# Kernel tuning notes

Measured on AMD Instinct MI355X. Metric: run time of the kernel, lower is better.

The kernel has to match this reference:

```python
import jax, jax.numpy as jnp
import numpy as np

NUM_HEADS = 16
EMBED = 1024
HEAD_DIM = EMBED // NUM_HEADS


def setup_inputs() -> dict:
    key = jax.random.key(0)
    k1, k2, k3, k4, k5 = jax.random.split(key, 5)
    B, N, D = 16, 1024, EMBED
    s_in = 1.0 / np.sqrt(D)
    x = jax.random.normal(k1, (B, N, D), dtype=jnp.float32)
    # Linear weights stored as [in, out] so y = x @ W + b (equiv to torch x @ W.T + b)
    W_qkv = jax.random.uniform(k2, (D, 3 * D), dtype=jnp.float32, minval=-s_in, maxval=s_in)
    b_qkv = jax.random.uniform(k3, (3 * D,), dtype=jnp.float32, minval=-s_in, maxval=s_in)
    W_fc = jax.random.uniform(k4, (D, D), dtype=jnp.float32, minval=-s_in, maxval=s_in)
    b_fc = jax.random.uniform(k5, (D,), dtype=jnp.float32, minval=-s_in, maxval=s_in)
    return {"x": x, "W_qkv": W_qkv, "b_qkv": b_qkv, "W_fc": W_fc, "b_fc": b_fc}


def reference(x, W_qkv, b_qkv, W_fc, b_fc):
    B, N, D = x.shape
    H, d_k = NUM_HEADS, HEAD_DIM
    qkv = x @ W_qkv + b_qkv                      # [B, N, 3D]
    qkv = qkv.reshape(B, N, 3, H, d_k)
    qkv = jnp.transpose(qkv, (2, 0, 3, 1, 4))    # [3, B, H, N, d_k]
    Q, K, V = qkv[0], qkv[1], qkv[2]
    scale = 1.0 / jnp.sqrt(jnp.asarray(d_k, dtype=x.dtype))
    scores = jnp.einsum("bhqd,bhkd->bhqk", Q, K) * scale
    attn = jax.nn.softmax(scores, axis=-1)       # dropout is identity in eval mode
    context = jnp.einsum("bhqk,bhkd->bhqd", attn, V)
    context = jnp.transpose(context, (0, 2, 1, 3)).reshape(B, N, D)
    return context @ W_fc + b_fc
```

## Files before the change

### kernel.cpp

```cpp
#include <hip/hip_runtime.h>
#include <cstdint>
#include <cstddef>

typedef unsigned short u16;
typedef __bf16 bf16_t;
typedef bf16_t bf16x8 __attribute__((ext_vector_type(8)));
typedef float f32x4 __attribute__((ext_vector_type(4)));

#define MFMA16(a, b, c) __builtin_amdgcn_mfma_f32_16x16x32_bf16((a), (b), (c), 0, 0, 0)
#define GLOBAL_AS __attribute__((address_space(1)))
#define LDS_AS __attribute__((address_space(3)))

#define SOFT_M 8.0f

__device__ __forceinline__ u16 f2bf(float f) {
    unsigned u = __float_as_uint(f);
    u += 0x7FFFu + ((u >> 16) & 1u);
    return (u16)(u >> 16);
}
__device__ __forceinline__ u16 f2bf_trunc(float f) {
    return (u16)(__float_as_uint(f) >> 16);
}
__device__ __forceinline__ void gll16(const u16* g, u16* l) {
    __builtin_amdgcn_global_load_lds((const GLOBAL_AS unsigned int*)g,
                                     (LDS_AS unsigned int*)l, 16, 0, 0);
}

__global__ __launch_bounds__(256) void conv_x_kernel(const float* __restrict__ x,
                                                     u16* __restrict__ xb) {
    int i = blockIdx.x * 256 + threadIdx.x;
    float4 v = ((const float4*)x)[i];
    ushort4 o;
    o.x = f2bf(v.x); o.y = f2bf(v.y); o.z = f2bf(v.z); o.w = f2bf(v.w);
    ((ushort4*)xb)[i] = o;
}

__global__ __launch_bounds__(256) void transpose_w_kernel(const float* __restrict__ W,
                                                          u16* __restrict__ Wt,
                                                          int R, int C) {
    __shared__ u16 tile[32][33];
    int c0 = blockIdx.x * 32, r0 = blockIdx.y * 32;
    int tx = threadIdx.x, ty = threadIdx.y;
#pragma unroll
    for (int i = 0; i < 4; i++)
        tile[ty + i * 8][tx] = f2bf(W[(size_t)(r0 + ty + i * 8) * C + c0 + tx]);
    __syncthreads();
#pragma unroll
    for (int i = 0; i < 4; i++)
        Wt[(size_t)(c0 + ty + i * 8) * R + r0 + tx] = tile[tx][ty + i * 8];
}

template <bool PROJ>
__global__ __launch_bounds__(512, 2) void gemm256_kernel(const u16* __restrict__ A,
                                                         const u16* __restrict__ Bt,
                                                         const float* __restrict__ bias,
                                                         u16* __restrict__ Qb,
                                                         u16* __restrict__ Kb,
                                                         u16* __restrict__ Vt,
                                                         float* __restrict__ outF) {
    __shared__ u16 lds[65536];
    u16* ldsA = lds;
    u16* ldsB = lds + 32768;

    int t = threadIdx.x;
    int lane = t & 63, wid = t >> 6;
    int lr = lane & 15, quad = lane >> 4;
    int m0 = blockIdx.x * 256, n0 = blockIdx.y * 256;
    int wmBase = (wid >> 2) * 128;
    int wnBase = (wid & 3) * 64;
    int kcol = (quad * 8) ^ (((lr >> 1) & 3) << 3);

    int srow = wid * 16 + (lane >> 2);
    int schk = ((lane & 3) ^ ((lane >> 3) & 3)) * 8;
    const u16* AgT = A + (size_t)(m0 + srow) * 1024 + schk;
    const u16* BgT = Bt + (size_t)(n0 + srow) * 1024 + schk;
    int dstOff = wid * 512;

    auto stageA = [&](int tt) {
        u16* d = ldsA + (tt & 3) * 8192 + dstOff;
        const u16* s = AgT + (size_t)tt * 32;
        gll16(s, d);
        gll16(s + 131072, d + 4096);
    };
    auto stageB = [&](int tt) {
        u16* d = ldsB + (tt & 3) * 8192 + dstOff;
        const u16* s = BgT + (size_t)tt * 32;
        gll16(s, d);
        gll16(s + 131072, d + 4096);
    };

    f32x4 acc[8][4];
    f32x4 zf = {0.f, 0.f, 0.f, 0.f};
#pragma unroll
    for (int i = 0; i < 8; i++)
#pragma unroll
        for (int j = 0; j < 4; j++) acc[i][j] = zf;

    stageA(0); stageB(0);
    stageA(1); stageB(1);
    asm volatile("s_waitcnt vmcnt(4)" ::: "memory");
    __builtin_amdgcn_s_barrier();
    __builtin_amdgcn_sched_barrier(0);

#pragma unroll 1
    for (int kt = 0; kt < 32; ++kt) {
        const u16* SA = ldsA + (kt & 3) * 8192;
        const u16* SB = ldsB + (kt & 3) * 8192;
        bf16x8 af[8];
#pragma unroll
        for (int mt = 0; mt < 8; mt++)
            af[mt] = *(const bf16x8*)&SA[(wmBase + mt * 16 + lr) * 32 + kcol];
        bf16x8 b0 = *(const bf16x8*)&SB[(wnBase + lr) * 32 + kcol];
        bf16x8 b1 = *(const bf16x8*)&SB[(wnBase + 16 + lr) * 32 + kcol];
        if (kt < 30) stageA(kt + 2);
        __builtin_amdgcn_s_barrier();
        __builtin_amdgcn_s_setprio(1);
#pragma unroll
        for (int mt = 0; mt < 8; mt++) {
            acc[mt][0] = MFMA16(af[mt], b0, acc[mt][0]);
            acc[mt][1] = MFMA16(af[mt], b1, acc[mt][1]);
        }
        __builtin_amdgcn_s_setprio(0);
        __builtin_amdgcn_s_barrier();
        bf16x8 b2 = *(const bf16x8*)&SB[(wnBase + 32 + lr) * 32 + kcol];
        bf16x8 b3 = *(const bf16x8*)&SB[(wnBase + 48 + lr) * 32 + kcol];
        if (kt < 30) stageB(kt + 2);
        __builtin_amdgcn_s_barrier();
        __builtin_amdgcn_s_setprio(1);
#pragma unroll
        for (int mt = 0; mt < 8; mt++) {
            acc[mt][2] = MFMA16(af[mt], b2, acc[mt][2]);
            acc[mt][3] = MFMA16(af[mt], b3, acc[mt][3]);
        }
        __builtin_amdgcn_s_setprio(0);
        if (kt <= 29)      asm volatile("s_waitcnt vmcnt(4)" ::: "memory");
        else if (kt == 30) asm volatile("s_waitcnt vmcnt(0)" ::: "memory");
        __builtin_amdgcn_s_barrier();
        __builtin_amdgcn_sched_barrier(0);
    }

    if constexpr (PROJ) {
#pragma unroll
        for (int nt = 0; nt < 4; nt++) {
            int col = n0 + wnBase + nt * 16 + lr;
            float bv = bias[col];
#pragma unroll
            for (int mt = 0; mt < 8; mt++) {
                f32x4 v = acc[mt][nt];
#pragma unroll
                for (int r = 0; r < 4; r++) {
                    int m = m0 + wmBase + mt * 16 + quad * 4 + r;
                    outF[(size_t)m * 1024 + col] = v[r] + bv;
                }
            }
        }
    } else {
        int s = n0 >> 10;
        if (s == 2) {
#pragma unroll
            for (int nt = 0; nt < 4; nt++) {
                int col = n0 + wnBase + nt * 16 + lr;
                int h = (col >> 6) & 15, d = col & 63;
                float bv = bias[col];
                int dsw = (d & 7) << 3;
#pragma unroll
                for (int mt = 0; mt < 8; mt++) {
                    f32x4 v = acc[mt][nt];
                    int mb = m0 + wmBase + mt * 16 + quad * 4;
                    int bb = mb >> 10, nn = mb & 1023;
                    int nn2 = (nn & ~63) | ((nn & 63) ^ dsw);
                    ushort4 o;
                    o.x = f2bf(v[0] + bv); o.y = f2bf(v[1] + bv);
                    o.z = f2bf(v[2] + bv); o.w = f2bf(v[3] + bv);
                    *(ushort4*)&Vt[(((size_t)(bb * 16 + h)) * 64 + d) * 1024 + nn2] = o;
                }
            }
        } else {
            u16* dst = (s == 0) ? Qb : Kb;
            float scale = (s == 0) ? 0.125f * 1.44269504089f : 1.0f;
#pragma unroll
            for (int nt = 0; nt < 4; nt++) {
                int col = n0 + wnBase + nt * 16 + lr;
                int h = (col >> 6) & 15, d = col & 63;
                float bv = bias[col];
#pragma unroll
                for (int mt = 0; mt < 8; mt++) {
                    f32x4 v = acc[mt][nt];
#pragma unroll
                    for (int r = 0; r < 4; r++) {
                        int m = m0 + wmBase + mt * 16 + quad * 4 + r;
                        int bb = m >> 10, nn = m & 1023;
                        int d2 = (s == 1) ? (d ^ ((nn & 7) << 3)) : d;
                        dst[(((size_t)(bb * 16 + h)) * 1024 + nn) * 64 + d2] =
                            f2bf((v[r] + bv) * scale);
                    }
                }
            }
        }
    }
}

__device__ __forceinline__ uint4 build_pa(f32x4 s0, f32x4 s1, float& lacc, bool qodd) {
    unsigned w[4];
    float part = 0.f;
#pragma unroll
    for (int half = 0; half < 2; half++) {
        unsigned lo = f2bf_trunc(__builtin_amdgcn_exp2f(s0[half * 2] - SOFT_M));
        unsigned hi = f2bf_trunc(__builtin_amdgcn_exp2f(s0[half * 2 + 1] - SOFT_M));
        part += __uint_as_float(lo << 16) + __uint_as_float(hi << 16);
        w[half] = lo | (hi << 16);
    }
#pragma unroll
    for (int half = 0; half < 2; half++) {
        unsigned lo = f2bf_trunc(__builtin_amdgcn_exp2f(s1[half * 2] - SOFT_M));
        unsigned hi = f2bf_trunc(__builtin_amdgcn_exp2f(s1[half * 2 + 1] - SOFT_M));
        part += __uint_as_float(lo << 16) + __uint_as_float(hi << 16);
        w[2 + half] = lo | (hi << 16);
    }
    lacc += part;
    unsigned x0 = qodd ? w[0] : w[2];
    unsigned x1 = qodd ? w[1] : w[3];
    unsigned y0 = __shfl_xor(x0, 16);
    unsigned y1 = __shfl_xor(x1, 16);
    uint4 r;
    r.x = qodd ? y0 : w[0];
    r.y = qodd ? y1 : w[1];
    r.z = qodd ? w[2] : y0;
    r.w = qodd ? w[3] : y1;
    return r;
}

__global__ __launch_bounds__(256, 4) void flash_attn_kernel(const u16* __restrict__ Qb,
                                                            const u16* __restrict__ Kb,
                                                            const u16* __restrict__ Vt,
                                                            u16* __restrict__ ctx) {
    __shared__ u16 smem[16384];
    u16* Ks0 = smem;
    u16* Vs0 = smem + 8192;
    int t = threadIdx.x, lane = t & 63, wid = t >> 6;
    int lr = lane & 15, quad = lane >> 4;
    int bh = blockIdx.x, q0 = blockIdx.y * 128;
    int b = bh >> 4, h = bh & 15;
    int xsw = (lr & 7) << 3;

    const u16* Kg = Kb + (size_t)bh * 65536;
    const u16* Vg = Vt + (size_t)bh * 65536;

#pragma unroll
    for (int i = 0; i < 2; i++) {
        gll16(Kg + wid * 1024 + i * 512 + lane * 8, Ks0 + wid * 1024 + i * 512);
        int row = wid * 16 + i * 8 + (lane >> 3);
        gll16(Vg + (size_t)row * 1024 + (lane & 7) * 8, Vs0 + wid * 1024 + i * 512);
    }

    const u16* Qw = Qb + ((size_t)bh * 1024 + q0 + wid * 32) * 64;
    bf16x8 qf[2][2];
#pragma unroll
    for (int mt = 0; mt < 2; mt++)
#pragma unroll
        for (int kk = 0; kk < 2; kk++)
            qf[mt][kk] = *(const bf16x8*)(Qw + (mt * 16 + lr) * 64 + kk * 32 + quad * 8);

    f32x4 oacc[2][4];
    f32x4 zf = {0.f, 0.f, 0.f, 0.f};
#pragma unroll
    for (int mt = 0; mt < 2; mt++)
#pragma unroll
        for (int dt = 0; dt < 4; dt++) oacc[mt][dt] = zf;
    float lsum0 = 0.f, lsum1 = 0.f;
    bool qodd = (quad & 1) != 0;
    int vperm8 = (((quad & 1) << 1) | (quad >> 1)) * 8;

    __syncthreads();

    for (int kt = 0; kt < 16; kt++) {
        int cur = kt & 1;
        if (kt < 15) {
            u16* kd = Ks0 + (cur ^ 1) * 4096;
            u16* vd = Vs0 + (cur ^ 1) * 4096;
            const u16* ks = Kg + (size_t)(kt + 1) * 4096;
#pragma unroll
            for (int i = 0; i < 2; i++) {
                gll16(ks + wid * 1024 + i * 512 + lane * 8, kd + wid * 1024 + i * 512);
                int row = wid * 16 + i * 8 + (lane >> 3);
                gll16(Vg + (size_t)row * 1024 + (kt + 1) * 64 + (lane & 7) * 8,
                      vd + wid * 1024 + i * 512);
            }
        }

        const u16* Kc = Ks0 + cur * 4096;
        f32x4 sc[2][4];
#pragma unroll
        for (int mt = 0; mt < 2; mt++)
#pragma unroll
            for (int nt = 0; nt < 4; nt++) sc[mt][nt] = zf;
#pragma unroll
        for (int nt = 0; nt < 4; nt++) {
            bf16x8 kf0 = *(const bf16x8*)&Kc[(nt * 16 + lr) * 64 + ((quad * 8) ^ xsw)];
            bf16x8 kf1 = *(const bf16x8*)&Kc[(nt * 16 + lr) * 64 + ((quad * 8 + 32) ^ xsw)];
#pragma unroll
            for (int mt = 0; mt < 2; mt++) {
                sc[mt][nt] = MFMA16(kf0, qf[mt][0], sc[mt][nt]);
                sc[mt][nt] = MFMA16(kf1, qf[mt][1], sc[mt][nt]);
            }
        }

        const u16* Vc = Vs0 + cur * 4096;
#pragma unroll
        for (int kc = 0; kc < 2; kc++) {
            uint4 pw0 = build_pa(sc[0][kc * 2], sc[0][kc * 2 + 1], lsum0, qodd);
            uint4 pw1 = build_pa(sc[1][kc * 2], sc[1][kc * 2 + 1], lsum1, qodd);
            bf16x8 pa0 = *(const bf16x8*)&pw0;
            bf16x8 pa1 = *(const bf16x8*)&pw1;
#pragma unroll
            for (int dt = 0; dt < 4; dt++) {
                bf16x8 vv = *(const bf16x8*)&Vc[(dt * 16 + lr) * 64 +
                                                ((kc * 32 + vperm8) ^ xsw)];
                oacc[0][dt] = MFMA16(pa0, vv, oacc[0][dt]);
                oacc[1][dt] = MFMA16(pa1, vv, oacc[1][dt]);
            }
        }

        __syncthreads();
    }

    u16* Ow = smem + wid * 2304;
#pragma unroll
    for (int mt = 0; mt < 2; mt++) {
        float lf = (mt == 0) ? lsum0 : lsum1;
        lf += __shfl_xor(lf, 16);
        lf += __shfl_xor(lf, 32);
        float inv = 1.0f / lf;
#pragma unroll
        for (int r = 0; r < 4; r++) {
            float invr = __shfl(inv, (lane & 48) | (quad * 4 + r));
#pragma unroll
            for (int dt = 0; dt < 4; dt++)
                Ow[(mt * 16 + quad * 4 + r) * 72 + dt * 16 + lr] =
                    f2bf(oacc[mt][dt][r] * invr);
        }
    }
#pragma unroll
    for (int j = 0; j < 4; j++) {
        int r2 = j * 8 + (lane >> 3);
        uint4 ov = *(const uint4*)&Ow[r2 * 72 + (lane & 7) * 8];
        int row = q0 + wid * 32 + r2;
        *(uint4*)&ctx[((size_t)b * 1024 + row) * 1024 + h * 64 + (lane & 7) * 8] = ov;
    }
}

extern "C" void kernel_launch(void* const* d_in, const int* in_sizes, int n_in,
                              void* d_out, int out_size, void* d_ws, size_t ws_size,
                              hipStream_t stream) {
    const float* x     = (const float*)d_in[0];
    const float* W_qkv = (const float*)d_in[1];
    const float* b_qkv = (const float*)d_in[2];
    const float* W_fc  = (const float*)d_in[3];
    const float* b_fc  = (const float*)d_in[4];
    float* out = (float*)d_out;
    char* ws = (char*)d_ws;

    u16* xb  = (u16*)(ws + 0);
    u16* wqt = (u16*)(ws + 33554432);
    u16* wft = (u16*)(ws + 39845888);
    u16* Qb  = (u16*)(ws + 41943040);
    u16* Kb  = (u16*)(ws + 75497472);
    u16* Vt  = (u16*)(ws + 109051904);
    u16* ctx = (u16*)(ws + 0);

    conv_x_kernel<<<16384, 256, 0, stream>>>(x, xb);
    transpose_w_kernel<<<dim3(96, 32), dim3(32, 8), 0, stream>>>(W_qkv, wqt, 1024, 3072);
    transpose_w_kernel<<<dim3(32, 32), dim3(32, 8), 0, stream>>>(W_fc, wft, 1024, 1024);
    gemm256_kernel<false><<<dim3(64, 12), 512, 0, stream>>>(xb, wqt, b_qkv,
                                                            Qb, Kb, Vt, nullptr);
    flash_attn_kernel<<<dim3(256, 8), 256, 0, stream>>>(Qb, Kb, Vt, ctx);
    gemm256_kernel<true><<<dim3(64, 4), 512, 0, stream>>>(ctx, wft, b_fc,
                                                          nullptr, nullptr, nullptr, out);
}
```

Measured before the change: 391.4 us.

## Deepen GEMM LDS prefetch to three stages and use one barrier per k-step

The bf16 GEMM main loop now keeps three k-tiles of global-to-LDS loads in flight instead of two, issuing both A and B stages for tile kt+3 at the top of each iteration. The split into two half-MFMA phases separated by three barriers is replaced by loading all four B fragments at once, running all 32 MFMAs, then one wait and one barrier per iteration. The vmcnt wait thresholds are adjusted to match the deeper ring. This aims to hide more global memory latency and cut synchronisation overhead, at the cost of more outstanding loads and slightly more register pressure for the extra B fragments.

```diff
diff --git a/kernel.cpp b/kernel.cpp
--- a/kernel.cpp
+++ b/kernel.cpp
@@ -98,42 +98,35 @@
 
     stageA(0); stageB(0);
     stageA(1); stageB(1);
-    asm volatile("s_waitcnt vmcnt(4)" ::: "memory");
+    stageA(2); stageB(2);
+    asm volatile("s_waitcnt vmcnt(8)" ::: "memory");
     __builtin_amdgcn_s_barrier();
     __builtin_amdgcn_sched_barrier(0);
 
 #pragma unroll 1
     for (int kt = 0; kt < 32; ++kt) {
+        if (kt <= 28) { stageA(kt + 3); stageB(kt + 3); }
+
         const u16* SA = ldsA + (kt & 3) * 8192;
         const u16* SB = ldsB + (kt & 3) * 8192;
-        bf16x8 af[8];
+        bf16x8 af[8], bfr[4];
 #pragma unroll
         for (int mt = 0; mt < 8; mt++)
             af[mt] = *(const bf16x8*)&SA[(wmBase + mt * 16 + lr) * 32 + kcol];
-        bf16x8 b0 = *(const bf16x8*)&SB[(wnBase + lr) * 32 + kcol];
-        bf16x8 b1 = *(const bf16x8*)&SB[(wnBase + 16 + lr) * 32 + kcol];
-        if (kt < 30) stageA(kt + 2);
-        __builtin_amdgcn_s_barrier();
+#pragma unroll
+        for (int nt = 0; nt < 4; nt++)
+            bfr[nt] = *(const bf16x8*)&SB[(wnBase + nt * 16 + lr) * 32 + kcol];
+
         __builtin_amdgcn_s_setprio(1);
 #pragma unroll
-        for (int mt = 0; mt < 8; mt++) {
-            acc[mt][0] = MFMA16(af[mt], b0, acc[mt][0]);
-            acc[mt][1] = MFMA16(af[mt], b1, acc[mt][1]);
-        }
+        for (int mt = 0; mt < 8; mt++)
+#pragma unroll
+            for (int nt = 0; nt < 4; nt++)
+                acc[mt][nt] = MFMA16(af[mt], bfr[nt], acc[mt][nt]);
         __builtin_amdgcn_s_setprio(0);
-        __builtin_amdgcn_s_barrier();
-        bf16x8 b2 = *(const bf16x8*)&SB[(wnBase + 32 + lr) * 32 + kcol];
-        bf16x8 b3 = *(const bf16x8*)&SB[(wnBase + 48 + lr) * 32 + kcol];
-        if (kt < 30) stageB(kt + 2);
-        __builtin_amdgcn_s_barrier();
-        __builtin_amdgcn_s_setprio(1);
-#pragma unroll
-        for (int mt = 0; mt < 8; mt++) {
-            acc[mt][2] = MFMA16(af[mt], b2, acc[mt][2]);
-            acc[mt][3] = MFMA16(af[mt], b3, acc[mt][3]);
-        }
-        __builtin_amdgcn_s_setprio(0);
-        if (kt <= 29)      asm volatile("s_waitcnt vmcnt(4)" ::: "memory");
+
+        if (kt <= 28)      asm volatile("s_waitcnt vmcnt(8)" ::: "memory");
+        else if (kt == 29) asm volatile("s_waitcnt vmcnt(4)" ::: "memory");
         else if (kt == 30) asm volatile("s_waitcnt vmcnt(0)" ::: "memory");
         __builtin_amdgcn_s_barrier();
         __builtin_amdgcn_sched_barrier(0);
```

Result: no change. 392.1 us (+0.2%).
